# Kernel tuning notes

Measured on AMD Instinct MI355X. Metric: run time of the kernel, lower is better.

Reference implementation:

```python
import jax, jax.numpy as jnp
import numpy as np
import math

B, S, D = 8, 1024, 1024
NH, NKV, HD = 16, 8, 64
BLK_NUM, BLK_SIZE = 128, 8

def apply_rope(x, cos, sin):
    # x: (B,S,H,HD); cos/sin: (S, HD//2)
    x1 = x[..., 0::2]
    x2 = x[..., 1::2]
    c = cos[None, :, None, :]
    s = sin[None, :, None, :]
    r1 = x1 * c - x2 * s
    r2 = x1 * s + x2 * c
    out = jnp.stack([r1, r2], axis=-1).reshape(x.shape)
    return out

def setup_inputs() -> dict:
    key = jax.random.key(0)
    ks = jax.random.split(key, 7)
    x = jax.random.normal(ks[0], (B, S, D), dtype=jnp.float32)
    scale = 1.0 / math.sqrt(D)
    wq = jax.random.normal(ks[1], (D, NH * HD), dtype=jnp.float32) * scale
    wk = jax.random.normal(ks[2], (D, NKV * HD), dtype=jnp.float32) * scale
    wv = jax.random.normal(ks[3], (D, NKV * HD), dtype=jnp.float32) * scale
    wo = jax.random.normal(ks[4], (NH * HD, D), dtype=jnp.float32) * scale
    pos = jnp.arange(S, dtype=jnp.float32)
    inv_freq = 1.0 / (10000.0 ** (jnp.arange(0, HD, 2, dtype=jnp.float32) / HD))
    ang = pos[:, None] * inv_freq[None, :]
    freqs_cis_cos = jnp.cos(ang)
    freqs_cis_sin = jnp.sin(ang)
    return {"x": x, "wq": wq, "wk": wk, "wv": wv, "wo": wo,
            "freqs_cis_cos": freqs_cis_cos, "freqs_cis_sin": freqs_cis_sin,
            "start_pos": 0}

def reference(x, wq, wk, wv, wo, freqs_cis_cos, freqs_cis_sin, start_pos):
    q = (x @ wq).reshape(B, S, NH, HD)
    k = (x @ wk).reshape(B, S, NKV, HD)
    v = (x @ wv).reshape(B, S, NKV, HD)
    q = apply_rope(q, freqs_cis_cos, freqs_cis_sin)
    k = apply_rope(k, freqs_cis_cos, freqs_cis_sin)
    # GQA: repeat kv heads
    rep = NH // NKV
    k = jnp.repeat(k, rep, axis=2)  # (B,S,NH,HD)
    v = jnp.repeat(v, rep, axis=2)
    # block-causal mask: q in block i attends to kv blocks j <= i
    blk_id = jnp.arange(S) // BLK_SIZE
    mask = blk_id[:, None] >= blk_id[None, :]  # (S,S)
    scores = jnp.einsum('bqhd,bkhd->bhqk', q, k) / math.sqrt(HD)
    scores = jnp.where(mask[None, None], scores, -jnp.inf)
    attn = jax.nn.softmax(scores, axis=-1)
    out = jnp.einsum('bhqk,bkhd->bqhd', attn, v).reshape(B, S, NH * HD)
    return out @ wo
```

## Files before the change

kernel.cpp:

```cpp
#include <hip/hip_runtime.h>
#include <cstdint>
#include <math.h>

#define B_   8
#define S_   1024
#define D_   1024
#define NH_  16
#define NKV_ 8
#define HD_  64
#define M_   (B_*S_)

using bf16   = __bf16;
using bf16x4 = __attribute__((ext_vector_type(4))) __bf16;
using bf16x8 = __attribute__((ext_vector_type(8))) __bf16;
using f32x4  = __attribute__((ext_vector_type(4))) float;

__device__ __forceinline__ void gll16(const bf16* g, const bf16* l) {
    __builtin_amdgcn_global_load_lds(
        (const __attribute__((address_space(1))) unsigned int*)(uintptr_t)g,
        (__attribute__((address_space(3))) unsigned int*)(uintptr_t)l,
        16, 0, 0);
}

__device__ __forceinline__ void vm_wait0()  { asm volatile("s_waitcnt vmcnt(0)" ::: "memory"); }
__device__ __forceinline__ void bar()       { __builtin_amdgcn_s_barrier(); asm volatile("" ::: "memory"); }

__global__ void k_cvt_bf16(const float* __restrict__ in, bf16* __restrict__ out, int n4) {
    int i = blockIdx.x * blockDim.x + threadIdx.x;
    if (i < n4) {
        float4 v = ((const float4*)in)[i];
        bf16x4 o = { (bf16)v.x, (bf16)v.y, (bf16)v.z, (bf16)v.w };
        ((bf16x4*)out)[i] = o;
    }
}

__global__ void k_transpose_all(const float* __restrict__ wq, const float* __restrict__ wk,
                                const float* __restrict__ wv, const float* __restrict__ wo,
                                bf16* __restrict__ wqkvT, bf16* __restrict__ woT) {
    __shared__ float tile[64 * 65];
    const int R = 1024;
    int bx = blockIdx.x;
    const float* in; bf16* out; int C, xo;
    if (bx < 16)      { in = wq; out = wqkvT;               C = 1024; xo = bx; }
    else if (bx < 24) { in = wk; out = wqkvT + 1024 * 1024; C = 512;  xo = bx - 16; }
    else if (bx < 32) { in = wv; out = wqkvT + 1536 * 1024; C = 512;  xo = bx - 24; }
    else              { in = wo; out = woT;                 C = 1024; xo = bx - 32; }
    int r0 = blockIdx.y * 64, c0 = xo * 64;
    int t = threadIdx.x;
    #pragma unroll
    for (int it = 0; it < 16; ++it) {
        int idx = it * 256 + t;
        int r = idx >> 6, c = idx & 63;
        tile[r * 65 + c] = in[(size_t)(r0 + r) * C + c0 + c];
    }
    __syncthreads();
    #pragma unroll
    for (int it = 0; it < 16; ++it) {
        int idx = it * 256 + t;
        int c = idx >> 6, r = idx & 63;
        out[(size_t)(c0 + c) * R + r0 + r] = (bf16)tile[r * 65 + c];
    }
}

template <typename OutT, int BN>
__global__ __launch_bounds__(512, 2) void k_gemm256(const bf16* __restrict__ A,
                                                    const bf16* __restrict__ Bt,
                                                    OutT* __restrict__ C, int M, int N, int K) {
    constexpr int NI = BN / 64;
    constexpr int NB = (BN * 8) / 512;
    __shared__ __align__(16) bf16 aLds[2 * 256 * 64];
    __shared__ __align__(16) bf16 bLds[2 * BN * 64];
    const int t    = threadIdx.x;
    const int lane = t & 63;
    const int w    = t >> 6;
    const int quad = lane >> 4;
    const int l16  = lane & 15;
    const int wr   = w >> 2;
    const int wc   = w & 3;
    const int m0 = blockIdx.y * 256;
    const int n0 = blockIdx.x * BN;

    f32x4 acc[8][NI] = {};

    auto stage = [&](int kb, int buf) {
        const int k0 = kb << 6;
        #pragma unroll
        for (int it = 0; it < 4; ++it) {
            int ci = it * 512 + t;
            int r = ci >> 3, c = ci & 7;
            int cg = c ^ (r & 7);
            gll16(A + (size_t)(m0 + r) * K + k0 + cg * 8, aLds + buf * (256 * 64) + ci * 8);
        }
        #pragma unroll
        for (int it = 0; it < NB; ++it) {
            int ci = it * 512 + t;
            int r = ci >> 3, c = ci & 7;
            int cg = c ^ (r & 7);
            gll16(Bt + (size_t)(n0 + r) * K + k0 + cg * 8, bLds + buf * (BN * 64) + ci * 8);
        }
    };

    const int NT = K >> 6;
    stage(0, 0);
    vm_wait0();
    bar();

    for (int T = 0; T < NT; ++T) {
        const int buf = T & 1;
        if (T + 1 < NT) stage(T + 1, buf ^ 1);

        const bf16* aL = aLds + buf * (256 * 64);
        const bf16* bL = bLds + buf * (BN * 64);
        #pragma unroll
        for (int kk = 0; kk < 2; ++kk) {
            bf16x8 af[8], bfr[NI];
            #pragma unroll
            for (int mi = 0; mi < 8; ++mi) {
                int row = wr * 128 + mi * 16 + l16;
                int ch  = (kk * 4 + quad) ^ (row & 7);
                af[mi] = *(const bf16x8*)&aL[row * 64 + ch * 8];
            }
            #pragma unroll
            for (int ni = 0; ni < NI; ++ni) {
                int row = wc * (NI * 16) + ni * 16 + l16;
                int ch  = (kk * 4 + quad) ^ (row & 7);
                bfr[ni] = *(const bf16x8*)&bL[row * 64 + ch * 8];
            }
            #pragma unroll
            for (int mi = 0; mi < 8; ++mi)
                #pragma unroll
                for (int ni = 0; ni < NI; ++ni)
                    acc[mi][ni] = __builtin_amdgcn_mfma_f32_16x16x32_bf16(af[mi], bfr[ni], acc[mi][ni], 0, 0, 0);
        }
        vm_wait0();
        bar();
    }

    #pragma unroll
    for (int mi = 0; mi < 8; ++mi)
        #pragma unroll
        for (int ni = 0; ni < NI; ++ni)
            #pragma unroll
            for (int r = 0; r < 4; ++r) {
                int row = m0 + wr * 128 + mi * 16 + quad * 4 + r;
                int col = n0 + wc * (NI * 16) + ni * 16 + l16;
                C[(size_t)row * N + col] = (OutT)acc[mi][ni][r];
            }
}

__global__ void k_rope(const bf16* __restrict__ qkv, const float* __restrict__ cosg,
                       const float* __restrict__ sing, bf16* __restrict__ qd, bf16* __restrict__ kd) {
    int token = blockIdx.x;
    int b = token >> 10, s = token & 1023;
    int t = threadIdx.x;
    int hh = t >> 3, i8 = t & 7;
    float4 c4 = *(const float4*)&cosg[s * 32 + i8 * 4];
    float4 s4 = *(const float4*)&sing[s * 32 + i8 * 4];
    int srcBase, dstBase;
    bf16* dst;
    float sf;
    if (hh < 16) {
        srcBase = token * 2048 + hh * 64;
        dstBase = ((b * NH_ + hh) * S_ + s) * 64;
        dst = qd;
        sf = 0.180336879f;
    } else {
        int h = hh - 16;
        srcBase = token * 2048 + 1024 + h * 64;
        dstBase = ((b * NKV_ + h) * S_ + s) * 64;
        dst = kd;
        sf = 1.0f;
    }
    bf16x8 v = *(const bf16x8*)&qkv[srcBase + i8 * 8];
    const float cc[4] = { c4.x, c4.y, c4.z, c4.w };
    const float ss[4] = { s4.x, s4.y, s4.z, s4.w };
    bf16x8 o;
    #pragma unroll
    for (int j = 0; j < 4; ++j) {
        float e  = (float)v[2 * j];
        float od = (float)v[2 * j + 1];
        o[2 * j]     = (bf16)(sf * (e * cc[j] - od * ss[j]));
        o[2 * j + 1] = (bf16)(sf * (e * ss[j] + od * cc[j]));
    }
    *(bf16x8*)&dst[dstBase + i8 * 8] = o;
}

__global__ void k_vtrans(const bf16* __restrict__ qkv, bf16* __restrict__ vt) {
    __shared__ __align__(16) bf16 tile[64 * 72];
    int bid = blockIdx.x;
    int st = bid & 15;
    int h  = (bid >> 4) & 7;
    int b  = bid >> 7;
    int s0 = st * 64;
    int t = threadIdx.x;
    #pragma unroll
    for (int it = 0; it < 2; ++it) {
        int ci = it * 256 + t;
        int r = ci >> 3, c = ci & 7;
        *(uint4*)&tile[r * 72 + c * 8] =
            *(const uint4*)&qkv[(size_t)(b * S_ + s0 + r) * 2048 + 1536 + h * 64 + c * 8];
    }
    __syncthreads();
    #pragma unroll
    for (int it = 0; it < 2; ++it) {
        int ci = it * 256 + t;
        int d = ci >> 3, sc = ci & 7;
        int g = sc >> 2, q4 = sc & 3;
        bf16x8 v;
        #pragma unroll
        for (int j = 0; j < 8; ++j) {
            int s_ext = g * 32 + q4 * 4 + (j & 3) + 16 * (j >> 2);
            v[j] = tile[s_ext * 72 + d];
        }
        *(bf16x8*)&vt[(size_t)((b * NKV_ + h) * 64 + d) * S_ + s0 + sc * 8] = v;
    }
}

__global__ __launch_bounds__(256) void k_attn(const bf16* __restrict__ q, const bf16* __restrict__ k,
                                              const bf16* __restrict__ vt, bf16* __restrict__ out) {
    __shared__ __align__(16) bf16 kt[2 * 64 * 64];
    __shared__ __align__(16) bf16 vtt[2 * 64 * 64];
    int bid = blockIdx.x;
    int pi = bid & 7;
    int h  = (bid >> 3) & 15;
    int b  = bid >> 7;
    int qtA = pi, qtB = 15 - pi;
    int hkv = h >> 1;
    int t = threadIdx.x;
    int w = t >> 6, lane = t & 63, quad = lane >> 4, l16 = lane & 15;

    const bf16* qh = q + (size_t)(b * NH_ + h) * S_ * 64;
    int qwA = qtA * 64 + w * 16, qwB = qtB * 64 + w * 16;
    const bf16* qbA = qh + (size_t)(qwA + l16) * 64;
    const bf16* qbB = qh + (size_t)(qwB + l16) * 64;
    bf16x8 qfA0 = *(const bf16x8*)(qbA + quad * 8);
    bf16x8 qfA1 = *(const bf16x8*)(qbA + 32 + quad * 8);
    bf16x8 qfB0 = *(const bf16x8*)(qbB + quad * 8);
    bf16x8 qfB1 = *(const bf16x8*)(qbB + 32 + quad * 8);

    const bf16* kg = k  + (size_t)(b * NKV_ + hkv) * S_ * 64;
    const bf16* vg = vt + (size_t)(b * NKV_ + hkv) * 64 * S_;

    const int sr0 = t >> 3;
    const int cs  = t & 7;

    auto stage = [&](int k0, int buf) {
        #pragma unroll
        for (int it = 0; it < 2; ++it) {
            int r  = sr0 + it * 32;
            int cg = cs ^ (r & 7);
            int ci = it * 256 + t;
            gll16(kg + (size_t)(k0 + r) * 64 + cg * 8, kt  + buf * 4096 + ci * 8);
            gll16(vg + (size_t)r * S_ + k0 + cg * 8,   vtt + buf * 4096 + ci * 8);
        }
    };

    const bf16 one = (bf16)1.0f;
    const bf16x8 vones = { one, one, one, one, one, one, one, one };

    f32x4 o[4] = {};
    f32x4 ol = {};
    bf16x8 qf0 = qfA0, qf1 = qfA1;
    int qw = qwA;

    auto epilogue = [&]() {
        #pragma unroll
        for (int r = 0; r < 4; ++r) {
            float invl = 1.0f / ol[r];
            #pragma unroll
            for (int dc = 0; dc < 4; ++dc) {
                int row = qw + quad * 4 + r;
                int col = h * 64 + dc * 16 + l16;
                out[(size_t)(b * S_ + row) * 1024 + col] = (bf16)(o[dc][r] * invl);
            }
        }
    };

    const int NU = 17;
    stage(0, 0);
    vm_wait0();
    bar();

    for (int u = 0; u < NU; ++u) {
        const int buf = u & 1;
        if (u + 1 < NU) {
            int un   = u + 1;
            int ktiN = (un > qtA) ? (un - qtA - 1) : un;
            stage(ktiN * 64, buf ^ 1);
        }
        int kti = (u > qtA) ? (u - qtA - 1) : u;
        int k0  = kti * 64;
        const bf16* ktb = kt  + buf * 4096;
        const bf16* vtb = vtt + buf * 4096;

        f32x4 sc[4] = {};
        #pragma unroll
        for (int kk = 0; kk < 2; ++kk)
            #pragma unroll
            for (int f = 0; f < 4; ++f) {
                int row = f * 16 + l16;
                int ch  = (kk * 4 + quad) ^ (row & 7);
                bf16x8 af = *(const bf16x8*)&ktb[row * 64 + ch * 8];
                sc[f] = __builtin_amdgcn_mfma_f32_16x16x32_bf16(af, kk ? qf1 : qf0, sc[f], 0, 0, 0);
            }

        bool diag = (u == qtA) || (u == NU - 1);
        int klim = ((qw + l16) & ~7) + 8;
        float p[4][4];
        #pragma unroll
        for (int f = 0; f < 4; ++f)
            #pragma unroll
            for (int r = 0; r < 4; ++r) {
                float pv = exp2f(sc[f][r]);
                if (diag && (k0 + f * 16 + quad * 4 + r >= klim)) pv = 0.f;
                p[f][r] = pv;
            }

        bf16x8 pa0, pa1;
        #pragma unroll
        for (int j = 0; j < 4; ++j) {
            pa0[j]     = (bf16)p[0][j];
            pa0[j + 4] = (bf16)p[1][j];
            pa1[j]     = (bf16)p[2][j];
            pa1[j + 4] = (bf16)p[3][j];
        }

        ol = __builtin_amdgcn_mfma_f32_16x16x32_bf16(pa0, vones, ol, 0, 0, 0);
        ol = __builtin_amdgcn_mfma_f32_16x16x32_bf16(pa1, vones, ol, 0, 0, 0);

        #pragma unroll
        for (int dc = 0; dc < 4; ++dc) {
            int row = dc * 16 + l16;
            #pragma unroll
            for (int kk = 0; kk < 2; ++kk) {
                int ch = (kk * 4 + quad) ^ (row & 7);
                bf16x8 vb = *(const bf16x8*)&vtb[row * 64 + ch * 8];
                o[dc] = __builtin_amdgcn_mfma_f32_16x16x32_bf16(kk ? pa1 : pa0, vb, o[dc], 0, 0, 0);
            }
        }

        if (u == qtA) {
            epilogue();
            #pragma unroll
            for (int dc = 0; dc < 4; ++dc) o[dc] = f32x4{0.f, 0.f, 0.f, 0.f};
            ol = f32x4{0.f, 0.f, 0.f, 0.f};
            qf0 = qfB0; qf1 = qfB1; qw = qwB;
        }

        vm_wait0();
        bar();
    }
    epilogue();
}

extern "C" void kernel_launch(void* const* d_in, const int* in_sizes, int n_in,
                              void* d_out, int out_size, void* d_ws, size_t ws_size,
                              hipStream_t stream) {
    const float* x  = (const float*)d_in[0];
    const float* wq = (const float*)d_in[1];
    const float* wk = (const float*)d_in[2];
    const float* wv = (const float*)d_in[3];
    const float* wo = (const float*)d_in[4];
    const float* fc = (const float*)d_in[5];
    const float* fs = (const float*)d_in[6];
    (void)in_sizes; (void)n_in; (void)out_size; (void)ws_size;

    char* ws = (char*)d_ws;
    bf16* xb    = (bf16*)(ws);
    bf16* wqkvT = (bf16*)(ws + (16u << 20));
    bf16* woT   = (bf16*)(ws + (20u << 20));
    bf16* qkvb  = (bf16*)(ws + (22u << 20));
    bf16* kb    = (bf16*)(ws + (54u << 20));
    bf16* vtb   = (bf16*)(ws + (62u << 20));
    bf16* qb    = xb;
    bf16* attnb = qkvb;

    k_cvt_bf16<<<dim3(8192), dim3(256), 0, stream>>>(x, xb, (M_ * D_) / 4);
    k_transpose_all<<<dim3(48, 16), dim3(256), 0, stream>>>(wq, wk, wv, wo, wqkvT, woT);

    k_gemm256<bf16, 256><<<dim3(8, 32), dim3(512), 0, stream>>>(xb, wqkvT, qkvb, M_, 2048, 1024);

    k_rope<<<dim3(8192), dim3(192), 0, stream>>>(qkvb, fc, fs, qb, kb);
    k_vtrans<<<dim3(1024), dim3(256), 0, stream>>>(qkvb, vtb);

    k_attn<<<dim3(1024), dim3(256), 0, stream>>>(qb, kb, vtb, attnb);

    k_gemm256<float, 128><<<dim3(8, 32), dim3(512), 0, stream>>>(attnb, woT, (float*)d_out, M_, 1024, 1024);
}
```

Before: 220.4 us.

## Merge prep kernels, pipeline GEMM phases, and split attention per query tile

Merges the convert and weight-transpose launches into one kernel, and the RoPE and V-transpose launches into another, which removes launch gaps. The GEMM now remaps block indices in a swizzled order for cache locality. Its K loop is split into four phases that interleave the next tile's A and B loads with MFMA work under raised wave priority. Attention moves from paired query tiles per block to one query tile per block, launched longest-first with a double-buffered unrolled loop and a hardware exp2 intrinsic. The trade-offs are extra barriers per K tile, a worse load balance from unpaired tiles, and the loss of exp2f's special-case handling.

```diff
diff --git a/kernel.cpp b/kernel.cpp
--- a/kernel.cpp
+++ b/kernel.cpp
@@ -25,28 +25,29 @@
 __device__ __forceinline__ void vm_wait0()  { asm volatile("s_waitcnt vmcnt(0)" ::: "memory"); }
 __device__ __forceinline__ void bar()       { __builtin_amdgcn_s_barrier(); asm volatile("" ::: "memory"); }
 
-__global__ void k_cvt_bf16(const float* __restrict__ in, bf16* __restrict__ out, int n4) {
-    int i = blockIdx.x * blockDim.x + threadIdx.x;
-    if (i < n4) {
-        float4 v = ((const float4*)in)[i];
+__global__ void k_prep1(const float* __restrict__ x,
+                        const float* __restrict__ wq, const float* __restrict__ wk,
+                        const float* __restrict__ wv, const float* __restrict__ wo,
+                        bf16* __restrict__ xb, bf16* __restrict__ wqkvT, bf16* __restrict__ woT) {
+    __shared__ float tile[64 * 65];
+    int bid = blockIdx.x;
+    int t = threadIdx.x;
+    if (bid < 8192) {
+        int i = bid * 256 + t;
+        float4 v = ((const float4*)x)[i];
         bf16x4 o = { (bf16)v.x, (bf16)v.y, (bf16)v.z, (bf16)v.w };
-        ((bf16x4*)out)[i] = o;
-    }
-}
-
-__global__ void k_transpose_all(const float* __restrict__ wq, const float* __restrict__ wk,
-                                const float* __restrict__ wv, const float* __restrict__ wo,
-                                bf16* __restrict__ wqkvT, bf16* __restrict__ woT) {
-    __shared__ float tile[64 * 65];
+        ((bf16x4*)xb)[i] = o;
+        return;
+    }
+    int b2 = bid - 8192;
+    int bx = b2 % 48, by = b2 / 48;
     const int R = 1024;
-    int bx = blockIdx.x;
     const float* in; bf16* out; int C, xo;
     if (bx < 16)      { in = wq; out = wqkvT;               C = 1024; xo = bx; }
     else if (bx < 24) { in = wk; out = wqkvT + 1024 * 1024; C = 512;  xo = bx - 16; }
     else if (bx < 32) { in = wv; out = wqkvT + 1536 * 1024; C = 512;  xo = bx - 24; }
     else              { in = wo; out = woT;                 C = 1024; xo = bx - 32; }
-    int r0 = blockIdx.y * 64, c0 = xo * 64;
-    int t = threadIdx.x;
+    int r0 = by * 64, c0 = xo * 64;
     #pragma unroll
     for (int it = 0; it < 16; ++it) {
         int idx = it * 256 + t;
@@ -77,12 +78,17 @@
     const int l16  = lane & 15;
     const int wr   = w >> 2;
     const int wc   = w & 3;
-    const int m0 = blockIdx.y * 256;
-    const int n0 = blockIdx.x * BN;
+
+    int bid = blockIdx.y * gridDim.x + blockIdx.x;
+    int cpx = (gridDim.x * gridDim.y) >> 3;
+    int sw  = (bid & 7) * cpx + (bid >> 3);
+    int bx  = sw % gridDim.x, by = sw / gridDim.x;
+    const int m0 = by * 256;
+    const int n0 = bx * BN;
 
     f32x4 acc[8][NI] = {};
 
-    auto stage = [&](int kb, int buf) {
+    auto stageA = [&](int kb, int buf) {
         const int k0 = kb << 6;
         #pragma unroll
         for (int it = 0; it < 4; ++it) {
@@ -91,6 +97,9 @@
             int cg = c ^ (r & 7);
             gll16(A + (size_t)(m0 + r) * K + k0 + cg * 8, aLds + buf * (256 * 64) + ci * 8);
         }
+    };
+    auto stageB = [&](int kb, int buf) {
+        const int k0 = kb << 6;
         #pragma unroll
         for (int it = 0; it < NB; ++it) {
             int ci = it * 512 + t;
@@ -101,39 +110,51 @@
     };
 
     const int NT = K >> 6;
-    stage(0, 0);
+
+    auto phase = [&](int buf, int kk, int mh, int stageSel, int nkb, bool lastInTile) {
+        const bf16* aL = aLds + buf * (256 * 64);
+        const bf16* bL = bLds + buf * (BN * 64);
+        bf16x8 af[4], bfr[NI];
+        #pragma unroll
+        for (int i = 0; i < 4; ++i) {
+            int row = wr * 128 + (mh * 4 + i) * 16 + l16;
+            int ch  = (kk * 4 + quad) ^ (row & 7);
+            af[i] = *(const bf16x8*)&aL[row * 64 + ch * 8];
+        }
+        #pragma unroll
+        for (int ni = 0; ni < NI; ++ni) {
+            int row = wc * (NI * 16) + ni * 16 + l16;
+            int ch  = (kk * 4 + quad) ^ (row & 7);
+            bfr[ni] = *(const bf16x8*)&bL[row * 64 + ch * 8];
+        }
+        if (stageSel == 1) stageA(nkb, buf ^ 1);
+        else if (stageSel == 2) stageB(nkb, buf ^ 1);
+        bar();
+        __builtin_amdgcn_s_setprio(1);
+        #pragma unroll
+        for (int i = 0; i < 4; ++i)
+            #pragma unroll
+            for (int ni = 0; ni < NI; ++ni)
+                acc[mh * 4 + i][ni] = __builtin_amdgcn_mfma_f32_16x16x32_bf16(af[i], bfr[ni], acc[mh * 4 + i][ni], 0, 0, 0);
+        __builtin_amdgcn_s_setprio(0);
+        if (lastInTile) vm_wait0();
+        bar();
+    };
+
+    auto doTile = [&](int T, int buf) {
+        bool hn = (T + 1 < NT);
+        phase(buf, 0, 0, hn ? 1 : 0, T + 1, false);
+        phase(buf, 0, 1, hn ? 2 : 0, T + 1, false);
+        phase(buf, 1, 0, 0, 0, false);
+        phase(buf, 1, 1, 0, 0, true);
+    };
+
+    stageA(0, 0); stageB(0, 0);
     vm_wait0();
     bar();
-
-    for (int T = 0; T < NT; ++T) {
-        const int buf = T & 1;
-        if (T + 1 < NT) stage(T + 1, buf ^ 1);
-
-        const bf16* aL = aLds + buf * (256 * 64);
-        const bf16* bL = bLds + buf * (BN * 64);
-        #pragma unroll
-        for (int kk = 0; kk < 2; ++kk) {
-            bf16x8 af[8], bfr[NI];
-            #pragma unroll
-            for (int mi = 0; mi < 8; ++mi) {
-                int row = wr * 128 + mi * 16 + l16;
-                int ch  = (kk * 4 + quad) ^ (row & 7);
-                af[mi] = *(const bf16x8*)&aL[row * 64 + ch * 8];
-            }
-            #pragma unroll
-            for (int ni = 0; ni < NI; ++ni) {
-                int row = wc * (NI * 16) + ni * 16 + l16;
-                int ch  = (kk * 4 + quad) ^ (row & 7);
-                bfr[ni] = *(const bf16x8*)&bL[row * 64 + ch * 8];
-            }
-            #pragma unroll
-            for (int mi = 0; mi < 8; ++mi)
-                #pragma unroll
-                for (int ni = 0; ni < NI; ++ni)
-                    acc[mi][ni] = __builtin_amdgcn_mfma_f32_16x16x32_bf16(af[mi], bfr[ni], acc[mi][ni], 0, 0, 0);
-        }
-        vm_wait0();
-        bar();
+    for (int T = 0; T < NT; T += 2) {
+        doTile(T, 0);
+        doTile(T + 1, 1);
     }
 
     #pragma unroll
@@ -148,51 +169,54 @@
             }
 }
 
-__global__ void k_rope(const bf16* __restrict__ qkv, const float* __restrict__ cosg,
-                       const float* __restrict__ sing, bf16* __restrict__ qd, bf16* __restrict__ kd) {
-    int token = blockIdx.x;
-    int b = token >> 10, s = token & 1023;
-    int t = threadIdx.x;
-    int hh = t >> 3, i8 = t & 7;
-    float4 c4 = *(const float4*)&cosg[s * 32 + i8 * 4];
-    float4 s4 = *(const float4*)&sing[s * 32 + i8 * 4];
-    int srcBase, dstBase;
-    bf16* dst;
-    float sf;
-    if (hh < 16) {
-        srcBase = token * 2048 + hh * 64;
-        dstBase = ((b * NH_ + hh) * S_ + s) * 64;
-        dst = qd;
-        sf = 0.180336879f;
-    } else {
-        int h = hh - 16;
-        srcBase = token * 2048 + 1024 + h * 64;
-        dstBase = ((b * NKV_ + h) * S_ + s) * 64;
-        dst = kd;
-        sf = 1.0f;
-    }
-    bf16x8 v = *(const bf16x8*)&qkv[srcBase + i8 * 8];
-    const float cc[4] = { c4.x, c4.y, c4.z, c4.w };
-    const float ss[4] = { s4.x, s4.y, s4.z, s4.w };
-    bf16x8 o;
-    #pragma unroll
-    for (int j = 0; j < 4; ++j) {
-        float e  = (float)v[2 * j];
-        float od = (float)v[2 * j + 1];
-        o[2 * j]     = (bf16)(sf * (e * cc[j] - od * ss[j]));
-        o[2 * j + 1] = (bf16)(sf * (e * ss[j] + od * cc[j]));
-    }
-    *(bf16x8*)&dst[dstBase + i8 * 8] = o;
-}
-
-__global__ void k_vtrans(const bf16* __restrict__ qkv, bf16* __restrict__ vt) {
+__global__ void k_prep2(const bf16* __restrict__ qkv, const float* __restrict__ cosg,
+                        const float* __restrict__ sing, bf16* __restrict__ qd,
+                        bf16* __restrict__ kd, bf16* __restrict__ vt) {
     __shared__ __align__(16) bf16 tile[64 * 72];
     int bid = blockIdx.x;
-    int st = bid & 15;
-    int h  = (bid >> 4) & 7;
-    int b  = bid >> 7;
+    int t = threadIdx.x;
+    if (bid < 8192) {
+        if (t < 192) {
+            int token = bid;
+            int b = token >> 10, s = token & 1023;
+            int hh = t >> 3, i8 = t & 7;
+            float4 c4 = *(const float4*)&cosg[s * 32 + i8 * 4];
+            float4 s4 = *(const float4*)&sing[s * 32 + i8 * 4];
+            int srcBase, dstBase;
+            bf16* dst;
+            float sf;
+            if (hh < 16) {
+                srcBase = token * 2048 + hh * 64;
+                dstBase = ((b * NH_ + hh) * S_ + s) * 64;
+                dst = qd;
+                sf = 0.180336879f;
+            } else {
+                int h = hh - 16;
+                srcBase = token * 2048 + 1024 + h * 64;
+                dstBase = ((b * NKV_ + h) * S_ + s) * 64;
+                dst = kd;
+                sf = 1.0f;
+            }
+            bf16x8 v = *(const bf16x8*)&qkv[srcBase + i8 * 8];
+            const float cc[4] = { c4.x, c4.y, c4.z, c4.w };
+            const float ss[4] = { s4.x, s4.y, s4.z, s4.w };
+            bf16x8 o;
+            #pragma unroll
+            for (int j = 0; j < 4; ++j) {
+                float e  = (float)v[2 * j];
+                float od = (float)v[2 * j + 1];
+                o[2 * j]     = (bf16)(sf * (e * cc[j] - od * ss[j]));
+                o[2 * j + 1] = (bf16)(sf * (e * ss[j] + od * cc[j]));
+            }
+            *(bf16x8*)&dst[dstBase + i8 * 8] = o;
+        }
+        return;
+    }
+    int b2 = bid - 8192;
+    int st = b2 & 15;
+    int h  = (b2 >> 4) & 7;
+    int b  = b2 >> 7;
     int s0 = st * 64;
-    int t = threadIdx.x;
     #pragma unroll
     for (int it = 0; it < 2; ++it) {
         int ci = it * 256 + t;
@@ -221,22 +245,18 @@
     __shared__ __align__(16) bf16 kt[2 * 64 * 64];
     __shared__ __align__(16) bf16 vtt[2 * 64 * 64];
     int bid = blockIdx.x;
-    int pi = bid & 7;
-    int h  = (bid >> 3) & 15;
-    int b  = bid >> 7;
-    int qtA = pi, qtB = 15 - pi;
+    int qt = 15 - (bid >> 7);
+    int combo = bid & 127;
+    int b = combo >> 4, h = combo & 15;
     int hkv = h >> 1;
     int t = threadIdx.x;
     int w = t >> 6, lane = t & 63, quad = lane >> 4, l16 = lane & 15;
 
     const bf16* qh = q + (size_t)(b * NH_ + h) * S_ * 64;
-    int qwA = qtA * 64 + w * 16, qwB = qtB * 64 + w * 16;
-    const bf16* qbA = qh + (size_t)(qwA + l16) * 64;
-    const bf16* qbB = qh + (size_t)(qwB + l16) * 64;
-    bf16x8 qfA0 = *(const bf16x8*)(qbA + quad * 8);
-    bf16x8 qfA1 = *(const bf16x8*)(qbA + 32 + quad * 8);
-    bf16x8 qfB0 = *(const bf16x8*)(qbB + quad * 8);
-    bf16x8 qfB1 = *(const bf16x8*)(qbB + 32 + quad * 8);
+    int qw = qt * 64 + w * 16;
+    const bf16* qb = qh + (size_t)(qw + l16) * 64;
+    bf16x8 qf0 = *(const bf16x8*)(qb + quad * 8);
+    bf16x8 qf1 = *(const bf16x8*)(qb + 32 + quad * 8);
 
     const bf16* kg = k  + (size_t)(b * NKV_ + hkv) * S_ * 64;
     const bf16* vg = vt + (size_t)(b * NKV_ + hkv) * 64 * S_;
@@ -244,7 +264,8 @@
     const int sr0 = t >> 3;
     const int cs  = t & 7;
 
-    auto stage = [&](int k0, int buf) {
+    auto stage = [&](int u, int buf) {
+        int k0 = u * 64;
         #pragma unroll
         for (int it = 0; it < 2; ++it) {
             int r  = sr0 + it * 32;
@@ -260,38 +281,12 @@
 
     f32x4 o[4] = {};
     f32x4 ol = {};
-    bf16x8 qf0 = qfA0, qf1 = qfA1;
-    int qw = qwA;
-
-    auto epilogue = [&]() {
-        #pragma unroll
-        for (int r = 0; r < 4; ++r) {
-            float invl = 1.0f / ol[r];
-            #pragma unroll
-            for (int dc = 0; dc < 4; ++dc) {
-                int row = qw + quad * 4 + r;
-                int col = h * 64 + dc * 16 + l16;
-                out[(size_t)(b * S_ + row) * 1024 + col] = (bf16)(o[dc][r] * invl);
-            }
-        }
-    };
-
-    const int NU = 17;
-    stage(0, 0);
-    vm_wait0();
-    bar();
-
-    for (int u = 0; u < NU; ++u) {
-        const int buf = u & 1;
-        if (u + 1 < NU) {
-            int un   = u + 1;
-            int ktiN = (un > qtA) ? (un - qtA - 1) : un;
-            stage(ktiN * 64, buf ^ 1);
-        }
-        int kti = (u > qtA) ? (u - qtA - 1) : u;
-        int k0  = kti * 64;
+    const int klim = ((qw + l16) & ~7) + 8;
+
+    auto unit = [&](int u, int buf, bool diag) {
         const bf16* ktb = kt  + buf * 4096;
         const bf16* vtb = vtt + buf * 4096;
+        int k0 = u * 64;
 
         f32x4 sc[4] = {};
         #pragma unroll
@@ -304,14 +299,12 @@
                 sc[f] = __builtin_amdgcn_mfma_f32_16x16x32_bf16(af, kk ? qf1 : qf0, sc[f], 0, 0, 0);
             }
 
-        bool diag = (u == qtA) || (u == NU - 1);
-        int klim = ((qw + l16) & ~7) + 8;
         float p[4][4];
         #pragma unroll
         for (int f = 0; f < 4; ++f)
             #pragma unroll
             for (int r = 0; r < 4; ++r) {
-                float pv = exp2f(sc[f][r]);
+                float pv = __builtin_amdgcn_exp2f(sc[f][r]);
                 if (diag && (k0 + f * 16 + quad * 4 + r >= klim)) pv = 0.f;
                 p[f][r] = pv;
             }
@@ -338,19 +331,34 @@
                 o[dc] = __builtin_amdgcn_mfma_f32_16x16x32_bf16(kk ? pa1 : pa0, vb, o[dc], 0, 0, 0);
             }
         }
-
-        if (u == qtA) {
-            epilogue();
-            #pragma unroll
-            for (int dc = 0; dc < 4; ++dc) o[dc] = f32x4{0.f, 0.f, 0.f, 0.f};
-            ol = f32x4{0.f, 0.f, 0.f, 0.f};
-            qf0 = qfB0; qf1 = qfB1; qw = qwB;
-        }
-
         vm_wait0();
         bar();
-    }
-    epilogue();
+    };
+
+    const int NU = qt + 1;
+    stage(0, 0);
+    vm_wait0();
+    bar();
+
+    int u = 0;
+    for (; u + 2 <= NU; u += 2) {
+        stage(u + 1, 1);
+        unit(u, 0, false);
+        if (u + 2 < NU) stage(u + 2, 0);
+        unit(u + 1, 1, (u + 1) == NU - 1);
+    }
+    if (u < NU) unit(u, 0, true);
+
+    #pragma unroll
+    for (int r = 0; r < 4; ++r) {
+        float invl = 1.0f / ol[r];
+        #pragma unroll
+        for (int dc = 0; dc < 4; ++dc) {
+            int row = qw + quad * 4 + r;
+            int col = h * 64 + dc * 16 + l16;
+            out[(size_t)(b * S_ + row) * 1024 + col] = (bf16)(o[dc][r] * invl);
+        }
+    }
 }
 
 extern "C" void kernel_launch(void* const* d_in, const int* in_sizes, int n_in,
@@ -375,15 +383,13 @@
     bf16* qb    = xb;
     bf16* attnb = qkvb;
 
-    k_cvt_bf16<<<dim3(8192), dim3(256), 0, stream>>>(x, xb, (M_ * D_) / 4);
-    k_transpose_all<<<dim3(48, 16), dim3(256), 0, stream>>>(wq, wk, wv, wo, wqkvT, woT);
+    k_prep1<<<dim3(8960), dim3(256), 0, stream>>>(x, wq, wk, wv, wo, xb, wqkvT, woT);
 
     k_gemm256<bf16, 256><<<dim3(8, 32), dim3(512), 0, stream>>>(xb, wqkvT, qkvb, M_, 2048, 1024);
 
-    k_rope<<<dim3(8192), dim3(192), 0, stream>>>(qkvb, fc, fs, qb, kb);
-    k_vtrans<<<dim3(1024), dim3(256), 0, stream>>>(qkvb, vtb);
-
-    k_attn<<<dim3(1024), dim3(256), 0, stream>>>(qb, kb, vtb, attnb);
+    k_prep2<<<dim3(9216), dim3(256), 0, stream>>>(qkvb, fc, fs, qb, kb, vtb);
+
+    k_attn<<<dim3(2048), dim3(256), 0, stream>>>(qb, kb, vtb, attnb);
 
     k_gemm256<float, 128><<<dim3(8, 32), dim3(512), 0, stream>>>(attnb, woT, (float*)d_out, M_, 1024, 1024);
 }
```

Measured after the change: 207.1 us. 6.0% less time.
